# Kernel tuning notes

Hardware: AMD Instinct MI355X
Metric: run time of the kernel (lower is better)

Reference implementation:

```python
import jax, jax.numpy as jnp
import numpy as np

N = 100000        # nodes
E_RAND = 1500000  # random edges (self loops appended -> E = 1.6M)
IN_DIM = 500
HID = 256
NCLASS = 50
K = 10


def setup_inputs() -> dict:
    key = jax.random.key(0)
    ks = jax.random.split(key, 8)
    feats = jax.random.normal(ks[0], (N, IN_DIM), dtype=jnp.float32)
    # edges: random + self loops (fit() adds self loops)
    src_r = jax.random.randint(ks[1], (E_RAND,), 0, N, dtype=jnp.int32)
    dst_r = jax.random.randint(ks[2], (E_RAND,), 0, N, dtype=jnp.int32)
    loop = jnp.arange(N, dtype=jnp.int32)
    src = jnp.concatenate([src_r, loop])
    dst = jnp.concatenate([dst_r, loop])
    # params (xavier-uniform-like scales)
    def xavier(k, shape):
        lim = np.sqrt(6.0 / (shape[0] + shape[1]))
        return jax.random.uniform(k, shape, jnp.float32, -lim, lim)
    W1 = xavier(ks[3], (IN_DIM, HID))
    b1 = jnp.zeros((HID,), jnp.float32)
    W2 = xavier(ks[4], (HID, NCLASS))
    b2 = jnp.zeros((NCLASS,), jnp.float32)
    s = xavier(ks[5], (NCLASS, 1))
    return {"feats": feats, "W1": W1, "b1": b1, "W2": W2, "b2": b2,
            "s": s, "src": src, "dst": dst}


def reference(feats, W1, b1, W2, b2, s, src, dst):
    # --- MLP (dropout is identity in eval / p=0) ---
    x = jax.nn.relu(feats @ W1 + b1)          # [N, HID]
    x = x @ W2 + b2                            # [N, NCLASS]
    # --- DAGNNConv: k-hop sym-normalized propagation ---
    deg = jax.ops.segment_sum(jnp.ones_like(dst, dtype=jnp.float32), dst,
                              num_segments=N)  # in-degrees
    norm = jnp.power(deg, -0.5)[:, None]       # [N, 1]
    results = [x]
    h = x
    for _ in range(K):
        h = h * norm
        h = jax.ops.segment_sum(h[src], dst, num_segments=N)  # copy_u + sum
        h = h * norm
        results.append(h)
    H = jnp.stack(results, axis=1)             # [N, K+1, C]
    S = jax.nn.sigmoid(jnp.einsum('nkc,co->nk', H, s))  # [N, K+1]
    out = jnp.einsum('nk,nkc->nc', S, H)       # [N, C]
    return out
```

## Files before the change

kernel.cpp:

```cpp
#include <hip/hip_runtime.h>
#include <hip/hip_bf16.h>
#include <math.h>

#define NN     100000
#define INDIM  500
#define HID    256
#define NCLASS 50
#define KHOPS  10
#define KPAD   512
#define CPAD   64

static inline size_t roundup256(size_t x) { return (x + 255) & ~(size_t)255; }

typedef __attribute__((ext_vector_type(8))) short bf16x8;
typedef __attribute__((ext_vector_type(4))) float f32x4;
typedef __attribute__((ext_vector_type(4))) short short4v;

typedef __attribute__((address_space(3))) unsigned       lds_u32;
typedef const __attribute__((address_space(1))) unsigned glb_u32;

__device__ inline short f2bf(float f) {
    union { float f; unsigned u; } v; v.f = f;
    unsigned r = v.u + 0x7FFFu + ((v.u >> 16) & 1u);
    return (short)(r >> 16);
}
__device__ inline short f2bf_hw(float f) {
    __hip_bfloat16 h = __float2bfloat16(f);
    return *reinterpret_cast<short*>(&h);
}
__device__ inline float bflo(unsigned u) {
    union { unsigned u; float f; } v; v.u = u << 16; return v.f;
}
__device__ inline float bfhi(unsigned u) {
    union { unsigned u; float f; } v; v.u = u & 0xFFFF0000u; return v.f;
}
__device__ inline unsigned packbf(float a, float b) {
    return (unsigned)(unsigned short)f2bf(a) | ((unsigned)(unsigned short)f2bf(b) << 16);
}

__global__ void dagnn_zero2(int* __restrict__ a, int* __restrict__ b, int n) {
    int i = blockIdx.x * blockDim.x + threadIdx.x;
    if (i < n) { a[i] = 0; b[i] = 0; }
}

__global__ void dagnn_deg(const int* __restrict__ dst, int* __restrict__ degi, int E) {
    int e = blockIdx.x * blockDim.x + threadIdx.x;
    if (e < E) atomicAdd(&degi[dst[e]], 1);
}

__global__ void dagnn_norm(const int* __restrict__ degi, float* __restrict__ nrm, int n) {
    int i = blockIdx.x * blockDim.x + threadIdx.x;
    if (i < n) nrm[i] = rsqrtf((float)degi[i]);
}

__global__ void dagnn_scan(const int* __restrict__ degi, int* __restrict__ rowptr, int n) {
    __shared__ int wsum[16];
    __shared__ int carry_s;
    const int tid  = threadIdx.x;
    const int lane = tid & 63;
    const int wid  = tid >> 6;
    if (tid == 0) carry_s = 0;
    __syncthreads();
    for (int base = 0; base < n; base += 4096) {
        int i0 = base + tid * 4;
        int v0 = (i0 + 0 < n) ? degi[i0 + 0] : 0;
        int v1 = (i0 + 1 < n) ? degi[i0 + 1] : 0;
        int v2 = (i0 + 2 < n) ? degi[i0 + 2] : 0;
        int v3 = (i0 + 3 < n) ? degi[i0 + 3] : 0;
        int tsum = v0 + v1 + v2 + v3;
        int x = tsum;
        #pragma unroll
        for (int off = 1; off < 64; off <<= 1) {
            int t = __shfl_up(x, off);
            if (lane >= off) x += t;
        }
        if (lane == 63) wsum[wid] = x;
        __syncthreads();
        if (tid == 0) {
            int run = carry_s;
            #pragma unroll
            for (int w = 0; w < 16; ++w) { int t = wsum[w]; wsum[w] = run; run += t; }
            carry_s = run;
        }
        __syncthreads();
        int texcl = wsum[wid] + (x - tsum);
        if (i0 + 0 < n) rowptr[i0 + 0] = texcl;
        if (i0 + 1 < n) rowptr[i0 + 1] = texcl + v0;
        if (i0 + 2 < n) rowptr[i0 + 2] = texcl + v0 + v1;
        if (i0 + 3 < n) rowptr[i0 + 3] = texcl + v0 + v1 + v2;
        __syncthreads();
    }
    if (tid == 0) rowptr[n] = carry_s;
}

__global__ void dagnn_fill(const int* __restrict__ src, const int* __restrict__ dst,
                           const int* __restrict__ rowptr, int* __restrict__ fillc,
                           int* __restrict__ colidx, int E) {
    int e = blockIdx.x * blockDim.x + threadIdx.x;
    if (e >= E) return;
    int d = dst[e];
    int pos = rowptr[d] + atomicAdd(&fillc[d], 1);
    colidx[pos] = src[e];
}

__global__ void dagnn_w1ts(const float* __restrict__ W1, short* __restrict__ Bts) {
    int idx = blockIdx.x * 256 + threadIdx.x;
    if (idx >= HID * KPAD) return;
    int ks = idx >> 13;
    int n  = (idx >> 5) & 255;
    int kk = idx & 31;
    int k  = ks * 32 + kk;
    float v = (k < INDIM) ? W1[(size_t)k * HID + n] : 0.f;
    Bts[idx] = f2bf(v);
}

__global__ void dagnn_w2t(const float* __restrict__ W2, short* __restrict__ W2t) {
    int idx = blockIdx.x * 256 + threadIdx.x;
    if (idx >= CPAD * HID) return;
    int n = idx >> 8;
    int k = idx & 255;
    float v = (n < NCLASS) ? W2[(size_t)k * NCLASS + n] : 0.f;
    W2t[idx] = f2bf(v);
}

__global__ void dagnn_sgate(const float* __restrict__ svec, float2* __restrict__ sg) {
    int c = threadIdx.x;
    if (c < 32) {
        float x = (2 * c     < NCLASS) ? svec[2 * c]     : 0.f;
        float y = (2 * c + 1 < NCLASS) ? svec[2 * c + 1] : 0.f;
        sg[c] = make_float2(x, y);
    }
}

#define G1_STAGE(ABASE, BBASE, KS)                                             \
    {                                                                          \
        const int k0_ = (KS) * 32;                                             \
        _Pragma("unroll")                                                      \
        for (int j = 0; j < 2; ++j) {                                          \
            int slot = (wid * 2 + j) * 64 + lane;                              \
            int mrow = slot >> 3;                                  \
            int q    = (slot & 7) ^ (mrow & 7);    \
            int gm   = row0 + mrow;                                            \
            int gk   = k0_ + q * 4;                                            \
            const float* asrc = (gm < M && gk < INDIM)                         \
                ? (A + (size_t)gm * INDIM + gk) : A;                           \
            __builtin_amdgcn_global_load_lds((glb_u32*)asrc,                   \
                (lds_u32*)((ABASE) + (wid * 2 + j) * 256), 16, 0, 0);          \
            const short* bsrc = Bts + ((size_t)(KS) << 13) + slot * 8;         \
            __builtin_amdgcn_global_load_lds((glb_u32*)bsrc,                   \
                (lds_u32*)((BBASE) + (wid * 2 + j) * 512), 16, 0, 0);          \
        }                                                                      \
    }

__global__ __launch_bounds__(512, 4) void dagnn_gemm1_mfma(
        const float* __restrict__ A, const short* __restrict__ Bts,
        const float* __restrict__ bias, short* __restrict__ C, int M) {
    __shared__ __align__(16) char smem[67584];
    float* As0 = (float*)smem;
    float* As1 = (float*)(smem + 16384);
    short* Bs0 = (short*)(smem + 32768);
    short* Bs1 = (short*)(smem + 49152);
    short* Ep  = (short*)smem;

    const int tid  = threadIdx.x;
    const int lane = tid & 63;
    const int wid  = tid >> 6;
    const int l16  = lane & 15;
    const int quad = lane >> 4;
    const int m_off = (wid & 1) * 64;
    const int n_off = (wid >> 1) * 64;
    const int row0  = blockIdx.x * 128;

    f32x4 acc[4][4] = {};

    G1_STAGE(As0, Bs0, 0)
    __syncthreads();

    for (int ks = 0; ks < KPAD / 32; ++ks) {
        const int cur = ks & 1;
        const float* ab = cur ? As1 : As0;
        const short* bb = cur ? Bs1 : Bs0;
        if (ks + 1 < KPAD / 32) {
            if (cur) { G1_STAGE(As0, Bs0, ks + 1) }
            else     { G1_STAGE(As1, Bs1, ks + 1) }
        }

        bf16x8 bfr[4];
        #pragma unroll
        for (int nt = 0; nt < 4; ++nt)
            bfr[nt] = *(const bf16x8*)(bb + (n_off + nt * 16 + l16) * 32 + quad * 8);

        #pragma unroll
        for (int mt = 0; mt < 4; ++mt) {
            int m  = m_off + mt * 16 + l16;
            int s0 = (quad * 2 + 0) ^ (m & 7);
            int s1 = (quad * 2 + 1) ^ (m & 7);
            float4 lo = *(const float4*)(ab + m * 32 + s0 * 4);
            float4 hi = *(const float4*)(ab + m * 32 + s1 * 4);
            bf16x8 af;
            af[0] = f2bf_hw(lo.x); af[1] = f2bf_hw(lo.y);
            af[2] = f2bf_hw(lo.z); af[3] = f2bf_hw(lo.w);
            af[4] = f2bf_hw(hi.x); af[5] = f2bf_hw(hi.y);
            af[6] = f2bf_hw(hi.z); af[7] = f2bf_hw(hi.w);
            #pragma unroll
            for (int nt = 0; nt < 4; ++nt)
                acc[mt][nt] = __builtin_amdgcn_mfma_f32_16x16x32_bf16(
                                  af, bfr[nt], acc[mt][nt], 0, 0, 0);
        }
        __syncthreads();
    }

    float bv[4];
    #pragma unroll
    for (int nt = 0; nt < 4; ++nt) bv[nt] = bias[n_off + nt * 16 + l16];

    #pragma unroll
    for (int mt = 0; mt < 4; ++mt) {
        #pragma unroll
        for (int nt = 0; nt < 4; ++nt) {
            #pragma unroll
            for (int r = 0; r < 4; ++r) {
                float v = acc[mt][nt][r] + bv[nt];
                v = v > 0.f ? v : 0.f;
                float vp = __shfl_xor(v, 1);
                if (!(l16 & 1)) {
                    int mrel = m_off + mt * 16 + quad * 4 + r;
                    *(unsigned*)(Ep + mrel * 264 + n_off + nt * 16 + l16) =
                        packbf(v, vp);
                }
            }
        }
    }
    __syncthreads();
    #pragma unroll
    for (int it = 0; it < 8; ++it) {
        int cidx = tid + it * 512;
        int rr   = cidx >> 5;
        int chk  = cidx & 31;
        int gm   = row0 + rr;
        if (gm < M)
            *(bf16x8*)(C + (size_t)gm * HID + chk * 8) =
                *(const bf16x8*)(Ep + rr * 264 + chk * 8);
    }
}

#define A2_STRIDE 72
#define B2_STRIDE 264
__global__ __launch_bounds__(256) void dagnn_mlp2_mfma(
        const short* __restrict__ hid, const short* __restrict__ W2t,
        const float* __restrict__ b2, const float* __restrict__ svec,
        const float* __restrict__ nrm,
        unsigned* __restrict__ hs0, float* __restrict__ out, int M) {
    __shared__ __align__(16) short As[128 * A2_STRIDE];
    __shared__ __align__(16) short Bs[CPAD * B2_STRIDE];

    const int tid  = threadIdx.x;
    const int lane = tid & 63;
    const int wid  = tid >> 6;
    const int l16  = lane & 15;
    const int quad = lane >> 4;
    const int m_off = wid * 32;
    const int row0  = blockIdx.x * 128;

    #pragma unroll
    for (int it = 0; it < 8; ++it) {
        int slot = tid + it * 256;
        int n   = slot >> 5;
        int seg = slot & 31;
        bf16x8 b = *(const bf16x8*)(W2t + (size_t)n * HID + seg * 8);
        *(bf16x8*)&Bs[n * B2_STRIDE + seg * 8] = b;
    }

    f32x4 acc[2][4] = {};

    for (int ks = 0; ks < HID / 64; ++ks) {
        const int k0 = ks * 64;
        #pragma unroll
        for (int it = 0; it < 4; ++it) {
            int slot = tid + it * 256;
            int m   = slot >> 3;
            int seg = slot & 7;
            int gm  = row0 + m;
            bf16x8 v = {};
            if (gm < M) v = *(const bf16x8*)(hid + (size_t)gm * HID + k0 + seg * 8);
            *(bf16x8*)&As[m * A2_STRIDE + seg * 8] = v;
        }
        __syncthreads();

        #pragma unroll
        for (int ksub = 0; ksub < 2; ++ksub) {
            bf16x8 af[2], bfr[4];
            #pragma unroll
            for (int mt = 0; mt < 2; ++mt)
                af[mt] = *(const bf16x8*)&As[(m_off + mt * 16 + l16) * A2_STRIDE
                                             + ksub * 32 + quad * 8];
            #pragma unroll
            for (int nt = 0; nt < 4; ++nt)
                bfr[nt] = *(const bf16x8*)&Bs[(nt * 16 + l16) * B2_STRIDE
                                              + k0 + ksub * 32 + quad * 8];
            #pragma unroll
            for (int mt = 0; mt < 2; ++mt)
                #pragma unroll
                for (int nt = 0; nt < 4; ++nt)
                    acc[mt][nt] = __builtin_amdgcn_mfma_f32_16x16x32_bf16(
                                      af[mt], bfr[nt], acc[mt][nt], 0, 0, 0);
        }
        __syncthreads();
    }

    float b2v[4], ssv[4];
    #pragma unroll
    for (int nt = 0; nt < 4; ++nt) {
        int gc = nt * 16 + l16;
        b2v[nt] = (gc < NCLASS) ? b2[gc]   : 0.f;
        ssv[nt] = (gc < NCLASS) ? svec[gc] : 0.f;
    }
    #pragma unroll
    for (int mt = 0; mt < 2; ++mt) {
        #pragma unroll
        for (int r = 0; r < 4; ++r) {
            int gm = row0 + m_off + mt * 16 + quad * 4 + r;
            float xv[4], q = 0.f;
            #pragma unroll
            for (int nt = 0; nt < 4; ++nt) {
                xv[nt] = acc[mt][nt][r] + b2v[nt];
                q += xv[nt] * ssv[nt];
            }
            #pragma unroll
            for (int off = 1; off < 16; off <<= 1) q += __shfl_xor(q, off);
            float S = 1.f / (1.f + __expf(-q));
            float nd = (gm < M) ? nrm[gm] : 0.f;
            #pragma unroll
            for (int nt = 0; nt < 4; ++nt) {
                int gc = nt * 16 + l16;
                float hv = xv[nt] * nd;
                float hp = __shfl_xor(hv, 1);
                if (gm < M) {
                    if (!(l16 & 1))
                        hs0[(size_t)gm * 32 + nt * 8 + (l16 >> 1)] = packbf(hv, hp);
                    if (gc < NCLASS) out[(size_t)gm * NCLASS + gc] = S * xv[nt];
                }
            }
        }
    }
}

__global__ __launch_bounds__(256) void dagnn_prop5(
        const unsigned* __restrict__ hs, const float* __restrict__ nrm,
        const int* __restrict__ rowptr, const int* __restrict__ colidx,
        const float2* __restrict__ sgate, unsigned* __restrict__ hs_next,
        float* __restrict__ out, int M, int write_next) {
    const int lane = threadIdx.x & 63;
    const int wid  = threadIdx.x >> 6;
    const int d    = blockIdx.x * 4 + wid;
    if (d >= M) return;
    const int half = lane >> 5;
    const int c    = lane & 31;
    const int beg = rowptr[d], end = rowptr[d + 1];
    const int deg = end - beg;
    const float nd = nrm[d];

    const int ch = 2 * c;
    float o0 = 0.f, o1 = 0.f;
    const bool ow = (half == 0) && (ch < NCLASS);
    if (ow) {
        o0 = out[(size_t)d * NCLASS + ch];
        o1 = out[(size_t)d * NCLASS + ch + 1];
    }

    int cv = (lane < deg) ? colidx[beg + lane] : 0;

    float a0 = 0.f, a1 = 0.f;
    const int dmain = deg > 64 ? 64 : deg;
    for (int i = 0; i < dmain; i += 16) {
        #pragma unroll
        for (int t = 0; t < 8; ++t) {
            int ei = i + half * 8 + t;
            int s = __shfl(cv, ei);
            if (ei < dmain) {
                unsigned u = hs[(size_t)s * 32 + c];
                a0 += bflo(u); a1 += bfhi(u);
            }
        }
    }
    for (int e = beg + 64; e + 2 <= end; e += 2) {
        int s = colidx[e + half];
        unsigned u = hs[(size_t)s * 32 + c];
        a0 += bflo(u); a1 += bfhi(u);
    }
    if (deg > 64 && ((deg - 64) & 1) && half == 0) {
        int s = colidx[end - 1];
        unsigned u = hs[(size_t)s * 32 + c];
        a0 += bflo(u); a1 += bfhi(u);
    }

    a0 += __shfl_xor(a0, 32);
    a1 += __shfl_xor(a1, 32);

    float r0 = a0 * nd, r1 = a1 * nd;
    float2 g = sgate[c];
    float p = r0 * g.x + r1 * g.y;
    #pragma unroll
    for (int off = 16; off; off >>= 1) p += __shfl_xor(p, off);
    float S = 1.f / (1.f + __expf(-p));
    if (half == 0) {
        if (write_next) hs_next[(size_t)d * 32 + c] = packbf(r0 * nd, r1 * nd);
        if (ch < NCLASS) {
            out[(size_t)d * NCLASS + ch]     = o0 + S * r0;
            out[(size_t)d * NCLASS + ch + 1] = o1 + S * r1;
        }
    }
}

extern "C" void kernel_launch(void* const* d_in, const int* in_sizes, int n_in,
                              void* d_out, int out_size, void* d_ws, size_t ws_size,
                              hipStream_t stream) {
    const float* feats = (const float*)d_in[0];
    const float* W1    = (const float*)d_in[1];
    const float* b1    = (const float*)d_in[2];
    const float* W2    = (const float*)d_in[3];
    const float* b2    = (const float*)d_in[4];
    const float* svec  = (const float*)d_in[5];
    const int*   src   = (const int*)d_in[6];
    const int*   dst   = (const int*)d_in[7];
    float* out = (float*)d_out;

    const int M = in_sizes[0] / INDIM;
    const int E = in_sizes[6];

    char* p = (char*)d_ws;
    size_t off = 0;
    short*    hid   = (short*)   (p + off); off += roundup256((size_t)M * HID * 2);
    unsigned* hsA   = (unsigned*)(p + off); off += roundup256((size_t)M * 32 * 4);
    unsigned* hsB   = (unsigned*)(p + off); off += roundup256((size_t)M * 32 * 4);
    short*    W1t   = (short*)   (p + off); off += roundup256((size_t)HID * KPAD * 2);
    short*    W2t   = (short*)   (p + off); off += roundup256((size_t)CPAD * HID * 2);
    float2*   sgate = (float2*)  (p + off); off += roundup256(32 * sizeof(float2));
    int*      degi  = (int*)     (p + off); off += roundup256((size_t)M * 4);
    float*    nrm   = (float*)   (p + off); off += roundup256((size_t)M * 4);
    int*      rowptr= (int*)     (p + off); off += roundup256((size_t)(M + 1) * 4);
    int*      fillc = (int*)     (p + off); off += roundup256((size_t)M * 4);
    int*      colidx= (int*)     (p + off); off += roundup256((size_t)E * 4);
    (void)ws_size;

    dagnn_zero2<<<(M + 255) / 256, 256, 0, stream>>>(degi, fillc, M);
    dagnn_deg<<<(E + 255) / 256, 256, 0, stream>>>(dst, degi, E);
    dagnn_norm<<<(M + 255) / 256, 256, 0, stream>>>(degi, nrm, M);
    dagnn_scan<<<1, 1024, 0, stream>>>(degi, rowptr, M);
    dagnn_fill<<<(E + 255) / 256, 256, 0, stream>>>(src, dst, rowptr, fillc, colidx, E);

    dagnn_w1ts<<<(HID * KPAD + 255) / 256, 256, 0, stream>>>(W1, W1t);
    dagnn_w2t<<<(CPAD * HID + 255) / 256, 256, 0, stream>>>(W2, W2t);
    dagnn_sgate<<<1, 32, 0, stream>>>(svec, sgate);

    dagnn_gemm1_mfma<<<(M + 127) / 128, 512, 0, stream>>>(feats, W1t, b1, hid, M);
    dagnn_mlp2_mfma<<<(M + 127) / 128, 256, 0, stream>>>(hid, W2t, b2, svec, nrm,
                                                         hsA, out, M);

    unsigned* hin = hsA;
    unsigned* hout = hsB;
    for (int k = 0; k < KHOPS; ++k) {
        dagnn_prop5<<<(M + 3) / 4, 256, 0, stream>>>(hin, nrm, rowptr, colidx,
                                                     sgate, hout, out, M,
                                                     k < KHOPS - 1);
        unsigned* t = hin; hin = hout; hout = t;
    }
}
```

Baseline: 1.287 ms.

## Split propagation into channel-group-major gathers and defer gating to a final pass

The bf16 hidden state moves from row-major (32 words per node) to four channel groups of 8 words each. Each propagation launch covers every node for all four groups, so each hop gathers from a smaller working set that fits in cache better. The per-hop sigmoid gate needs all channels, so each hop writes its fp32 results and partial gate dot products to a large workspace, and a new final kernel applies the sigmoid gating and accumulates into out. This trades the per-hop read-modify-write of out for extra workspace traffic and a final reduction pass, and it gathers 32-byte segments instead of 128-byte rows.

```diff
diff --git a/kernel.cpp b/kernel.cpp
--- a/kernel.cpp
+++ b/kernel.cpp
@@ -337,7 +337,8 @@
                 float hp = __shfl_xor(hv, 1);
                 if (gm < M) {
                     if (!(l16 & 1))
-                        hs0[(size_t)gm * 32 + nt * 8 + (l16 >> 1)] = packbf(hv, hp);
+                        hs0[(size_t)nt * M * 8 + (size_t)gm * 8 + (l16 >> 1)] =
+                            packbf(hv, hp);
                     if (gc < NCLASS) out[(size_t)gm * NCLASS + gc] = S * xv[nt];
                 }
             }
@@ -345,71 +346,77 @@
     }
 }
 
-__global__ __launch_bounds__(256) void dagnn_prop5(
+__global__ __launch_bounds__(256) void dagnn_propg(
         const unsigned* __restrict__ hs, const float* __restrict__ nrm,
         const int* __restrict__ rowptr, const int* __restrict__ colidx,
         const float2* __restrict__ sgate, unsigned* __restrict__ hs_next,
-        float* __restrict__ out, int M, int write_next) {
+        float* __restrict__ rbuf, float* __restrict__ pp, int M, int nb) {
+    const int wid  = threadIdx.x >> 6;
     const int lane = threadIdx.x & 63;
+    const int g    = blockIdx.x / nb;
+    const int bb   = blockIdx.x - g * nb;
+    const int d    = bb * 4 + wid;
+    if (d >= M) return;
+    const int e8 = lane >> 3;
+    const int j  = lane & 7;
+    const int beg = rowptr[d];
+    const int deg = rowptr[d + 1] - beg;
+    const float nd = nrm[d];
+    const unsigned* hsg = hs + (size_t)g * M * 8;
+
+    float a0 = 0.f, a1 = 0.f;
+    int sA = -1;
+    if (e8 < deg) sA = __builtin_nontemporal_load(&colidx[beg + e8]);
+    for (int i = 0; i < deg; i += 8) {
+        int sB = -1;
+        int nx = i + 8 + e8;
+        if (nx < deg) sB = __builtin_nontemporal_load(&colidx[beg + nx]);
+        if (sA >= 0) {
+            unsigned u = hsg[(size_t)sA * 8 + j];
+            a0 += bflo(u); a1 += bfhi(u);
+        }
+        sA = sB;
+    }
+    #pragma unroll
+    for (int off = 8; off < 64; off <<= 1) {
+        a0 += __shfl_xor(a0, off);
+        a1 += __shfl_xor(a1, off);
+    }
+    float r0 = a0 * nd, r1 = a1 * nd;
+    float2 gt = sgate[g * 8 + j];
+    float q = r0 * gt.x + r1 * gt.y;
+    #pragma unroll
+    for (int off = 1; off < 8; off <<= 1) q += __shfl_xor(q, off);
+
+    if (lane < 8) {
+        unsigned pk = packbf(r0 * nd, r1 * nd);
+        __builtin_nontemporal_store(pk,
+            &hs_next[(size_t)g * M * 8 + (size_t)d * 8 + j]);
+        __builtin_nontemporal_store(r0, &rbuf[(size_t)d * 64 + g * 16 + 2 * j]);
+        __builtin_nontemporal_store(r1, &rbuf[(size_t)d * 64 + g * 16 + 2 * j + 1]);
+        if (j == 0)
+            __builtin_nontemporal_store(q, &pp[(size_t)d * 4 + g]);
+    }
+}
+
+__global__ __launch_bounds__(256) void dagnn_final(
+        const float* __restrict__ rbuf, const float* __restrict__ pp,
+        float* __restrict__ out, int M) {
     const int wid  = threadIdx.x >> 6;
-    const int d    = blockIdx.x * 4 + wid;
+    const int lane = threadIdx.x & 63;
+    const int d = blockIdx.x * 4 + wid;
     if (d >= M) return;
-    const int half = lane >> 5;
-    const int c    = lane & 31;
-    const int beg = rowptr[d], end = rowptr[d + 1];
-    const int deg = end - beg;
-    const float nd = nrm[d];
-
-    const int ch = 2 * c;
-    float o0 = 0.f, o1 = 0.f;
-    const bool ow = (half == 0) && (ch < NCLASS);
-    if (ow) {
-        o0 = out[(size_t)d * NCLASS + ch];
-        o1 = out[(size_t)d * NCLASS + ch + 1];
-    }
-
-    int cv = (lane < deg) ? colidx[beg + lane] : 0;
-
-    float a0 = 0.f, a1 = 0.f;
-    const int dmain = deg > 64 ? 64 : deg;
-    for (int i = 0; i < dmain; i += 16) {
-        #pragma unroll
-        for (int t = 0; t < 8; ++t) {
-            int ei = i + half * 8 + t;
-            int s = __shfl(cv, ei);
-            if (ei < dmain) {
-                unsigned u = hs[(size_t)s * 32 + c];
-                a0 += bflo(u); a1 += bfhi(u);
-            }
-        }
-    }
-    for (int e = beg + 64; e + 2 <= end; e += 2) {
-        int s = colidx[e + half];
-        unsigned u = hs[(size_t)s * 32 + c];
-        a0 += bflo(u); a1 += bfhi(u);
-    }
-    if (deg > 64 && ((deg - 64) & 1) && half == 0) {
-        int s = colidx[end - 1];
-        unsigned u = hs[(size_t)s * 32 + c];
-        a0 += bflo(u); a1 += bfhi(u);
-    }
-
-    a0 += __shfl_xor(a0, 32);
-    a1 += __shfl_xor(a1, 32);
-
-    float r0 = a0 * nd, r1 = a1 * nd;
-    float2 g = sgate[c];
-    float p = r0 * g.x + r1 * g.y;
-    #pragma unroll
-    for (int off = 16; off; off >>= 1) p += __shfl_xor(p, off);
-    float S = 1.f / (1.f + __expf(-p));
-    if (half == 0) {
-        if (write_next) hs_next[(size_t)d * 32 + c] = packbf(r0 * nd, r1 * nd);
-        if (ch < NCLASS) {
-            out[(size_t)d * NCLASS + ch]     = o0 + S * r0;
-            out[(size_t)d * NCLASS + ch + 1] = o1 + S * r1;
-        }
-    }
+    float acc = 0.f;
+    #pragma unroll
+    for (int k = 0; k < KHOPS; ++k) {
+        const float4 pv = *(const float4*)&pp[(size_t)k * M * 4 + (size_t)d * 4];
+        float p = (pv.x + pv.y) + (pv.z + pv.w);
+        float S = 1.f / (1.f + __expf(-p));
+        float r = rbuf[(size_t)k * M * 64 + (size_t)d * 64 + lane];
+        acc += S * r;
+    }
+    if (lane < NCLASS)
+        out[(size_t)d * NCLASS + lane] += acc;
 }
 
 extern "C" void kernel_launch(void* const* d_in, const int* in_sizes, int n_in,
@@ -441,6 +448,8 @@
     int*      rowptr= (int*)     (p + off); off += roundup256((size_t)(M + 1) * 4);
     int*      fillc = (int*)     (p + off); off += roundup256((size_t)M * 4);
     int*      colidx= (int*)     (p + off); off += roundup256((size_t)E * 4);
+    float*    rbuf  = (float*)   (p + off); off += roundup256((size_t)KHOPS * M * 64 * 4);
+    float*    pp    = (float*)   (p + off); off += roundup256((size_t)KHOPS * M * 4 * 4);
     (void)ws_size;
 
     dagnn_zero2<<<(M + 255) / 256, 256, 0, stream>>>(degi, fillc, M);
@@ -457,12 +466,16 @@
     dagnn_mlp2_mfma<<<(M + 127) / 128, 256, 0, stream>>>(hid, W2t, b2, svec, nrm,
                                                          hsA, out, M);
 
+    const int nb = (M + 3) / 4;
     unsigned* hin = hsA;
     unsigned* hout = hsB;
     for (int k = 0; k < KHOPS; ++k) {
-        dagnn_prop5<<<(M + 3) / 4, 256, 0, stream>>>(hin, nrm, rowptr, colidx,
-                                                     sgate, hout, out, M,
-                                                     k < KHOPS - 1);
+        dagnn_propg<<<4 * nb, 256, 0, stream>>>(hin, nrm, rowptr, colidx, sgate,
+                                                hout,
+                                                rbuf + (size_t)k * M * 64,
+                                                pp   + (size_t)k * M * 4,
+                                                M, nb);
         unsigned* t = hin; hin = hout; hout = t;
     }
-}
+    dagnn_final<<<(M + 3) / 4, 256, 0, stream>>>(rbuf, pp, out, M);
+}
```

New measurement: 2.286 ms. +77.7%, slower.
